# Kernel optimization log

Measured on AMD Instinct MI355X. Metric: run time of the kernel, lower is better.

Reference implementation:

```python
import jax, jax.numpy as jnp
import numpy as np

N_NODES, N_EDGES, N_GRAPHS = 20000, 320000, 8
NFD, HID, OUT, HEADS = 128, 64, 768, 4


def gat_conv(x, src, dst, ea, W, att_src, att_dst, We, att_edge, bias, heads, concat):
    """PyG GATConv with edge_dim, add_self_loops=True (fill_value='mean'), eval mode."""
    N = x.shape[0]
    H = heads
    C = W.shape[1] // H
    loop = jnp.arange(N, dtype=src.dtype)
    s = jnp.concatenate([src, loop])
    d = jnp.concatenate([dst, loop])
    ea_full = jnp.concatenate([ea, jnp.broadcast_to(ea.mean(axis=0), (N, ea.shape[1]))], axis=0)
    h = (x @ W).reshape(N, H, C)                      # [N,H,C]
    a_s = (h * att_src).sum(-1)                        # [N,H]
    a_d = (h * att_dst).sum(-1)                        # [N,H]
    eh = (ea_full @ We).reshape(-1, H, C)              # [Etot,H,C]
    a_e = (eh * att_edge).sum(-1)                      # [Etot,H]
    logit = jax.nn.leaky_relu(a_s[s] + a_d[d] + a_e, negative_slope=0.2)
    m = jax.ops.segment_max(logit, d, num_segments=N)  # segment softmax over dst
    w = jnp.exp(logit - m[d])
    z = jax.ops.segment_sum(w, d, num_segments=N)
    alpha = w / (z[d] + 1e-16)                         # [Etot,H]
    out = jax.ops.segment_sum(h[s] * alpha[:, :, None], d, num_segments=N)
    out = out.reshape(N, H * C) if concat else out.mean(axis=1)
    return out + bias


def setup_inputs() -> dict:
    key = jax.random.key(0)
    ks = jax.random.split(key, 32)
    p = lambda k, shp: (jax.random.normal(k, shp) * 0.1).astype(jnp.float32)
    inp = {
        'x': jax.random.normal(ks[0], (N_NODES, 5), dtype=jnp.float32),
        'edge_index': jax.random.randint(ks[1], (2, N_EDGES), 0, N_NODES, dtype=jnp.int32),
        'edge_attr': jax.random.uniform(ks[2], (N_EDGES, 4), dtype=jnp.float32),
        'batch': jnp.sort(jax.random.randint(ks[3], (N_NODES,), 0, N_GRAPHS, dtype=jnp.int32)),
        # node_encoder
        'enc_w1': p(ks[4], (5, NFD // 2)), 'enc_b1': jnp.zeros((NFD // 2,), jnp.float32),
        'enc_w2': p(ks[5], (NFD // 2, NFD)), 'enc_b2': jnp.zeros((NFD,), jnp.float32),
        # gat1: in NFD -> HEADS*HID (concat)
        'g1_w': p(ks[6], (NFD, HEADS * HID)), 'g1_asrc': p(ks[7], (HEADS, HID)),
        'g1_adst': p(ks[8], (HEADS, HID)), 'g1_we': p(ks[9], (4, HEADS * HID)),
        'g1_aedge': p(ks[10], (HEADS, HID)), 'g1_b': jnp.zeros((HEADS * HID,), jnp.float32),
        # gat2: in HEADS*HID -> HEADS*HID (concat)
        'g2_w': p(ks[11], (HEADS * HID, HEADS * HID)), 'g2_asrc': p(ks[12], (HEADS, HID)),
        'g2_adst': p(ks[13], (HEADS, HID)), 'g2_we': p(ks[14], (4, HEADS * HID)),
        'g2_aedge': p(ks[15], (HEADS, HID)), 'g2_b': jnp.zeros((HEADS * HID,), jnp.float32),
        # gat3: in HEADS*HID -> HID, heads=1, concat=False
        'g3_w': p(ks[16], (HEADS * HID, HID)), 'g3_asrc': p(ks[17], (1, HID)),
        'g3_adst': p(ks[18], (1, HID)), 'g3_we': p(ks[19], (4, HID)),
        'g3_aedge': p(ks[20], (1, HID)), 'g3_b': jnp.zeros((HID,), jnp.float32),
        # projection HID -> 2*HID -> OUT
        'proj_w1': p(ks[21], (HID, 2 * HID)), 'proj_b1': jnp.zeros((2 * HID,), jnp.float32),
        'proj_w2': p(ks[22], (2 * HID, OUT)), 'proj_b2': jnp.zeros((OUT,), jnp.float32),
        # 5 vulnerability heads stacked: OUT -> 5
        'vuln_w': p(ks[23], (OUT, 5)), 'vuln_b': jnp.zeros((5,), jnp.float32),
    }
    return inp


def reference(x, edge_index, edge_attr, batch,
              enc_w1, enc_b1, enc_w2, enc_b2,
              g1_w, g1_asrc, g1_adst, g1_we, g1_aedge, g1_b,
              g2_w, g2_asrc, g2_adst, g2_we, g2_aedge, g2_b,
              g3_w, g3_asrc, g3_adst, g3_we, g3_aedge, g3_b,
              proj_w1, proj_b1, proj_w2, proj_b2, vuln_w, vuln_b):
    src, dst = edge_index[0], edge_index[1]
    # node_encoder (eval mode, dropout = identity)
    h = jax.nn.relu(x @ enc_w1 + enc_b1)
    h = jax.nn.relu(h @ enc_w2 + enc_b2)                         # [N, NFD]
    # EdgeAwareGAT
    h = jax.nn.elu(gat_conv(h, src, dst, edge_attr, g1_w, g1_asrc, g1_adst, g1_we, g1_aedge, g1_b, HEADS, True))
    h = jax.nn.elu(gat_conv(h, src, dst, edge_attr, g2_w, g2_asrc, g2_adst, g2_we, g2_aedge, g2_b, HEADS, True))
    h = gat_conv(h, src, dst, edge_attr, g3_w, g3_asrc, g3_adst, g3_we, g3_aedge, g3_b, 1, False)  # [N, HID]
    # global_mean_pool
    sums = jax.ops.segment_sum(h, batch, num_segments=N_GRAPHS)
    cnts = jax.ops.segment_sum(jnp.ones((h.shape[0], 1), h.dtype), batch, num_segments=N_GRAPHS)
    g = sums / jnp.maximum(cnts, 1.0)                            # [B, HID]
    # projection
    p1 = jax.nn.relu(g @ proj_w1 + proj_b1)
    static_features = p1 @ proj_w2 + proj_b2                     # [B, OUT]
    scores = jax.nn.sigmoid(static_features @ vuln_w + vuln_b)   # [B, 5]
    return static_features, scores
```

## Files before the change

### kernel.cpp

```cpp
#include <hip/hip_runtime.h>
#include <hip/hip_bf16.h>
#include <hip/hip_fp16.h>
#include <math.h>

#define N_NODES 20000
#define M_PAD 20096
#define N_EDGES 320000
#define N_GRAPHS 8

typedef _Float16 half8 __attribute__((ext_vector_type(8)));
typedef float floatx4 __attribute__((ext_vector_type(4)));

struct h4pack { __half2 a, b; };

__device__ __forceinline__ float leaky02(float x) { return x > 0.f ? x : 0.2f * x; }
__device__ __forceinline__ float sel4(int hl, float a, float b, float c, float d) {
    return hl < 2 ? (hl == 0 ? a : b) : (hl == 2 ? c : d);
}

__global__ void encoder_kernel(const float* __restrict__ x,
                               const float* __restrict__ w1, const float* __restrict__ b1,
                               const float* __restrict__ w2, const float* __restrict__ b2,
                               __half* __restrict__ out) {
    const int n0 = blockIdx.x * 8;
    const int tid = threadIdx.x;
    __shared__ float s_x[8][5];
    __shared__ float s_h1[8][64];
    if (tid < 40) s_x[tid / 5][tid % 5] = x[(size_t)(n0 + tid / 5) * 5 + (tid % 5)];
    __syncthreads();
    if (tid < 64) {
        #pragma unroll
        for (int n = 0; n < 8; ++n) {
            float a = b1[tid];
            #pragma unroll
            for (int k = 0; k < 5; ++k) a += s_x[n][k] * w1[k * 64 + tid];
            s_h1[n][tid] = fmaxf(a, 0.f);
        }
    }
    __syncthreads();
    float acc[8];
    #pragma unroll
    for (int n = 0; n < 8; ++n) acc[n] = b2[tid];
    for (int k = 0; k < 64; ++k) {
        float wv = w2[k * 128 + tid];
        #pragma unroll
        for (int n = 0; n < 8; ++n) acc[n] += s_h1[n][k] * wv;
    }
    #pragma unroll
    for (int n = 0; n < 8; ++n)
        out[(size_t)(n0 + n) * 128 + tid] = __float2half(fmaxf(acc[n], 0.f));
}

__global__ void prep_kernel(const float* __restrict__ ea, const int* __restrict__ dst,
                            float* __restrict__ ea_sum, int* __restrict__ cnt) {
    const int tid = threadIdx.x;
    float a0 = 0, a1 = 0, a2 = 0, a3 = 0;
    for (int i = blockIdx.x * blockDim.x + tid; i < N_EDGES; i += gridDim.x * blockDim.x) {
        float4 v = ((const float4*)ea)[i];
        a0 += v.x; a1 += v.y; a2 += v.z; a3 += v.w;
        atomicAdd(&cnt[dst[i]], 1);
    }
    #pragma unroll
    for (int off = 32; off; off >>= 1) {
        a0 += __shfl_down(a0, off, 64);
        a1 += __shfl_down(a1, off, 64);
        a2 += __shfl_down(a2, off, 64);
        a3 += __shfl_down(a3, off, 64);
    }
    __shared__ float s[4][4];
    const int wave = tid >> 6, lane = tid & 63;
    if (lane == 0) { s[wave][0] = a0; s[wave][1] = a1; s[wave][2] = a2; s[wave][3] = a3; }
    __syncthreads();
    if (tid < 4) {
        float t = s[0][tid] + s[1][tid] + s[2][tid] + s[3][tid];
        atomicAdd(&ea_sum[tid], t);
    }
}

__global__ void scan_kernel(const int* __restrict__ cnt, int* __restrict__ row_ptr) {
    __shared__ int s_sum[1024];
    const int tid = threadIdx.x;
    int local[20];
    int run = 0;
    const int base = tid * 20;
    #pragma unroll
    for (int i = 0; i < 20; ++i) {
        int idx = base + i;
        int v = (idx < N_NODES) ? cnt[idx] : 0;
        run += v;
        local[i] = run;
    }
    s_sum[tid] = run;
    __syncthreads();
    for (int off = 1; off < 1024; off <<= 1) {
        int v = (tid >= off) ? s_sum[tid - off] : 0;
        __syncthreads();
        s_sum[tid] += v;
        __syncthreads();
    }
    const int prev = (tid > 0) ? s_sum[tid - 1] : 0;
    #pragma unroll
    for (int i = 0; i < 20; ++i) {
        int idx = base + i;
        if (idx < N_NODES) row_ptr[idx + 1] = prev + local[i];
    }
    if (tid == 0) row_ptr[0] = 0;
}

__global__ void scatter_kernel(const int* __restrict__ src, const int* __restrict__ dst,
                               const float* __restrict__ ea,
                               const int* __restrict__ row_ptr, int* __restrict__ cur,
                               int* __restrict__ csr_src, float* __restrict__ csr_ea) {
    int i = blockIdx.x * 256 + threadIdx.x;
    if (i < N_EDGES) {
        int d = dst[i];
        int p = atomicAdd(&cur[d], 1);
        int idx = row_ptr[d] + p;
        csr_src[idx] = src[i];
        ((float4*)csr_ea)[idx] = ((const float4*)ea)[i];
    }
}

__global__ void const_prep_kernel(const float* __restrict__ w1, const float* __restrict__ w2,
                                  const float* __restrict__ w3,
                                  __half* __restrict__ wt1, __half* __restrict__ wt2,
                                  __half* __restrict__ wt3,
                                  const float* __restrict__ we1, const float* __restrict__ ae1,
                                  const float* __restrict__ we2, const float* __restrict__ ae2,
                                  const float* __restrict__ we3, const float* __restrict__ ae3,
                                  const float* __restrict__ ea_sum,
                                  float* __restrict__ vtab, float* __restrict__ lpae) {
    const int b = blockIdx.x;
    if (b < 448) {
        int i = b * 256 + threadIdx.x;
        if (i < 32768) {
            int k = i >> 8, n = i & 255;
            wt1[(size_t)n * 128 + k] = __float2half(w1[i]);
        } else if (i < 98304) {
            int j = i - 32768;
            int k = j >> 8, n = j & 255;
            wt2[(size_t)n * 256 + k] = __float2half(w2[j]);
        } else if (i < 114688) {
            int j = i - 98304;
            int k = j >> 6, n = j & 63;
            wt3[(size_t)n * 256 + k] = __float2half(w3[j]);
        }
        return;
    }
    const int L = b - 448;
    const float* We = (L == 0) ? we1 : ((L == 1) ? we2 : we3);
    const float* Ae = (L == 0) ? ae1 : ((L == 1) ? ae2 : ae3);
    const int H = (L < 2) ? 4 : 1;
    const int tid = threadIdx.x;
    __shared__ float s_v[16];
    if (tid < 4 * H) {
        const int k = tid / H, h = tid % H;
        float v = 0.f;
        for (int c = 0; c < 64; ++c) v += We[k * (H * 64) + h * 64 + c] * Ae[h * 64 + c];
        vtab[L * 16 + k * 4 + h] = v;
        s_v[k * 4 + h] = v;
    }
    __syncthreads();
    if (tid < H) {
        const float inv = 1.0f / (float)N_EDGES;
        float l = 0.f;
        #pragma unroll
        for (int k = 0; k < 4; ++k) l += ea_sum[k] * inv * s_v[k * 4 + tid];
        lpae[L * 4 + tid] = l;
    }
}

template<int N, int H>
__global__ __launch_bounds__(256) void mgemm_kernel(
    const __half* __restrict__ X, const __half* __restrict__ Wt,
    const float* __restrict__ asrc, const float* __restrict__ adst,
    __half* __restrict__ Y, float* __restrict__ a_s, float* __restrict__ a_d, int K) {
    constexpr int STR = 72;
    __shared__ _Float16 sX[64 * STR];
    __shared__ _Float16 sW[64 * STR];
    const int tid = threadIdx.x;
    const int lane = tid & 63, w = tid >> 6;
    const int l16 = lane & 15, kg = lane >> 4;
    const int n0 = blockIdx.x * 64;
    const int c0 = blockIdx.y * 64;
    const int by = blockIdx.y;

    floatx4 acc[4];
    #pragma unroll
    for (int ct = 0; ct < 4; ++ct) acc[ct] = (floatx4){0.f, 0.f, 0.f, 0.f};

    const int srow = tid >> 2, sseg = tid & 3;
    for (int k0 = 0; k0 < K; k0 += 64) {
        float4 xv0 = *(const float4*)(X + (size_t)(n0 + srow) * K + k0 + sseg * 8);
        float4 xv1 = *(const float4*)(X + (size_t)(n0 + srow) * K + k0 + 32 + sseg * 8);
        float4 wv0 = *(const float4*)(Wt + (size_t)(c0 + srow) * K + k0 + sseg * 8);
        float4 wv1 = *(const float4*)(Wt + (size_t)(c0 + srow) * K + k0 + 32 + sseg * 8);
        __syncthreads();
        *(float4*)&sX[srow * STR + sseg * 8] = xv0;
        *(float4*)&sX[srow * STR + 32 + sseg * 8] = xv1;
        *(float4*)&sW[srow * STR + sseg * 8] = wv0;
        *(float4*)&sW[srow * STR + 32 + sseg * 8] = wv1;
        __syncthreads();
        #pragma unroll
        for (int ks = 0; ks < 2; ++ks) {
            half8 a = *(const half8*)&sX[(w * 16 + l16) * STR + ks * 32 + kg * 8];
            #pragma unroll
            for (int ct = 0; ct < 4; ++ct) {
                half8 b = *(const half8*)&sW[(ct * 16 + l16) * STR + ks * 32 + kg * 8];
                acc[ct] = __builtin_amdgcn_mfma_f32_16x16x32_f16(a, b, acc[ct], 0, 0, 0);
            }
        }
    }

    const int rowb = n0 + w * 16 + kg * 4;
    float ar[4], ad4[4];
    #pragma unroll
    for (int ct = 0; ct < 4; ++ct) {
        ar[ct] = asrc[c0 + ct * 16 + l16];
        ad4[ct] = adst[c0 + ct * 16 + l16];
    }
    #pragma unroll
    for (int ct = 0; ct < 4; ++ct) {
        const int col = c0 + ct * 16 + l16;
        #pragma unroll
        for (int r = 0; r < 4; ++r)
            Y[(size_t)(rowb + r) * N + col] = __float2half(acc[ct][r]);
    }
    #pragma unroll
    for (int r = 0; r < 4; ++r) {
        float p = acc[0][r] * ar[0] + acc[1][r] * ar[1] + acc[2][r] * ar[2] + acc[3][r] * ar[3];
        float q = acc[0][r] * ad4[0] + acc[1][r] * ad4[1] + acc[2][r] * ad4[2] + acc[3][r] * ad4[3];
        #pragma unroll
        for (int off = 1; off < 16; off <<= 1) {
            p += __shfl_xor(p, off, 64);
            q += __shfl_xor(q, off, 64);
        }
        if (l16 == 0) {
            const int node = rowb + r;
            a_s[(size_t)node * H + by] = p;
            a_d[(size_t)node * H + by] = q;
        }
    }
}

template<int H, int HC, bool ELU>
__global__ __launch_bounds__(256) void agg4_kernel(
    const __half* __restrict__ hh,
    const float* __restrict__ a_s, const float* __restrict__ a_d,
    const float* __restrict__ vtab, const float* __restrict__ lpae,
    const int* __restrict__ csr_src, const float* __restrict__ csr_ea,
    const int* __restrict__ row_ptr, const float* __restrict__ bias,
    __half* __restrict__ out) {
    constexpr int CPT = HC / 64;
    const int wave = threadIdx.x >> 6;
    const int lane = threadIdx.x & 63;
    const int d = blockIdx.x * 4 + wave;

    const int base = row_ptr[d], end = row_ptr[d + 1];
    const int colbase = lane * CPT;
    const int hl = (H == 1) ? 0 : (colbase >> 6);

    float vt[4][H];
    #pragma unroll
    for (int k = 0; k < 4; ++k)
        #pragma unroll
        for (int h = 0; h < H; ++h) vt[k][h] = vtab[k * 4 + h];

    float add_[H], lself[H];
    if (H == 4) {
        float4 t = *(const float4*)&a_d[(size_t)d * 4];
        add_[0] = t.x; add_[1] = t.y; add_[2] = t.z; add_[3] = t.w;
        float4 s4 = *(const float4*)&a_s[(size_t)d * 4];
        lself[0] = leaky02(s4.x + add_[0] + lpae[0]);
        lself[1] = leaky02(s4.y + add_[1] + lpae[1]);
        lself[2] = leaky02(s4.z + add_[2] + lpae[2]);
        lself[3] = leaky02(s4.w + add_[3] + lpae[3]);
    } else {
        add_[0] = a_d[d];
        lself[0] = leaky02(a_s[d] + add_[0] + lpae[0]);
    }

    float zacc = 1.f;
    float acc[CPT];
    if (CPT == 4) {
        h4pack hv = *(const h4pack*)(hh + (size_t)d * HC + colbase);
        float2 f0 = __half22float2(hv.a);
        float2 f1 = __half22float2(hv.b);
        acc[0] = f0.x; acc[1] = f0.y; acc[2] = f1.x; acc[3] = f1.y;
    } else {
        acc[0] = __half2float(hh[(size_t)d * HC + colbase]);
    }

#define EDGE_STEP(tt) { \
        int s_ = __shfl(my_s, (tt), 64); \
        float w_; \
        if (H == 4) { \
            float t0 = __shfl(w0, (tt), 64), t1 = __shfl(w1, (tt), 64); \
            float t2 = __shfl(w2, (tt), 64), t3 = __shfl(w3, (tt), 64); \
            w_ = sel4(hl, t0, t1, t2, t3); \
        } else { \
            w_ = __shfl(w0, (tt), 64); \
        } \
        if (CPT == 4) { \
            h4pack hv_ = *(const h4pack*)(hh + (size_t)s_ * HC + colbase); \
            float2 f0_ = __half22float2(hv_.a); \
            float2 f1_ = __half22float2(hv_.b); \
            acc[0] += w_ * f0_.x; acc[1] += w_ * f0_.y; \
            acc[2] += w_ * f1_.x; acc[3] += w_ * f1_.y; \
        } else { \
            acc[0] += w_ * __half2float(hh[(size_t)s_ * HC + colbase]); \
        } \
        zacc += w_; }

    for (int c0 = base; c0 < end; c0 += 64) {
        const int nc = min(64, end - c0);
        int my_s = 0;
        float w0 = 0.f, w1 = 0.f, w2 = 0.f, w3 = 0.f;
        if (lane < nc) {
            my_s = csr_src[c0 + lane];
            float4 eav = ((const float4*)csr_ea)[c0 + lane];
            if (H == 4) {
                float4 as4 = *(const float4*)&a_s[(size_t)my_s * 4];
                float l0 = leaky02(as4.x + add_[0] + eav.x * vt[0][0] + eav.y * vt[1][0] + eav.z * vt[2][0] + eav.w * vt[3][0]);
                float l1 = leaky02(as4.y + add_[1] + eav.x * vt[0][1] + eav.y * vt[1][1] + eav.z * vt[2][1] + eav.w * vt[3][1]);
                float l2 = leaky02(as4.z + add_[2] + eav.x * vt[0][2] + eav.y * vt[1][2] + eav.z * vt[2][2] + eav.w * vt[3][2]);
                float l3 = leaky02(as4.w + add_[3] + eav.x * vt[0][3] + eav.y * vt[1][3] + eav.z * vt[2][3] + eav.w * vt[3][3]);
                w0 = __expf(l0 - lself[0]);
                w1 = __expf(l1 - lself[1]);
                w2 = __expf(l2 - lself[2]);
                w3 = __expf(l3 - lself[3]);
            } else {
                float l0 = leaky02(a_s[my_s] + add_[0] + eav.x * vt[0][0] + eav.y * vt[1][0] + eav.z * vt[2][0] + eav.w * vt[3][0]);
                w0 = __expf(l0 - lself[0]);
            }
        }
        int t = 0;
        for (; t + 8 <= nc; t += 8) {
            EDGE_STEP(t)
            EDGE_STEP(t + 1)
            EDGE_STEP(t + 2)
            EDGE_STEP(t + 3)
            EDGE_STEP(t + 4)
            EDGE_STEP(t + 5)
            EDGE_STEP(t + 6)
            EDGE_STEP(t + 7)
        }
        for (; t < nc; ++t) {
            EDGE_STEP(t)
        }
    }
#undef EDGE_STEP

    const float invz = 1.f / (zacc + 1e-16f);
    #pragma unroll
    for (int c = 0; c < CPT; ++c) {
        float v = acc[c] * invz + bias[colbase + c];
        if (ELU) v = (v > 0.f) ? v : (__expf(v) - 1.f);
        acc[c] = v;
    }
    if (CPT == 4) {
        __half2* op = (__half2*)(out + (size_t)d * HC + colbase);
        op[0] = __floats2half2_rn(acc[0], acc[1]);
        op[1] = __floats2half2_rn(acc[2], acc[3]);
    } else {
        out[(size_t)d * HC + colbase] = __float2half(acc[0]);
    }
}

__global__ void pool_kernel(const __half* __restrict__ h3, const int* __restrict__ batch,
                            float* __restrict__ psum, float* __restrict__ pcnt) {
    __shared__ float s_acc[8][64];
    __shared__ float s_cnt[8];
    const int tid = threadIdx.x;
    for (int i = tid; i < 512; i += 256) s_acc[i >> 6][i & 63] = 0.f;
    if (tid < 8) s_cnt[tid] = 0.f;
    __syncthreads();
    const int col = tid & 63, nl = tid >> 6;
    const int n0 = blockIdx.x * 64;
    for (int nn = nl; nn < 64; nn += 4) {
        int n = n0 + nn;
        if (n < N_NODES) {
            int b = batch[n];
            atomicAdd(&s_acc[b][col], __half2float(h3[(size_t)n * 64 + col]));
            if (col == 0) atomicAdd(&s_cnt[b], 1.0f);
        }
    }
    __syncthreads();
    for (int i = tid; i < 512; i += 256) {
        float v = s_acc[i >> 6][i & 63];
        if (v != 0.f) atomicAdd(&psum[i], v);
    }
    if (tid < 8 && s_cnt[tid] > 0.f) atomicAdd(&pcnt[tid], s_cnt[tid]);
}

__global__ void head_sf_kernel(const float* __restrict__ psum, const float* __restrict__ pcnt,
                               const float* __restrict__ w1, const float* __restrict__ b1,
                               const float* __restrict__ w2, const float* __restrict__ b2,
                               float* __restrict__ out) {
    const int b = blockIdx.y;
    const int c0 = blockIdx.x * 128;
    const int tid = threadIdx.x;
    __shared__ float s_g[64];
    __shared__ float s_p1[128];
    if (tid < 64) {
        float c = pcnt[b];
        c = (c < 1.f) ? 1.f : c;
        s_g[tid] = psum[b * 64 + tid] / c;
    }
    __syncthreads();
    {
        float a = b1[tid];
        #pragma unroll 8
        for (int k = 0; k < 64; ++k) a += s_g[k] * w1[k * 128 + tid];
        s_p1[tid] = fmaxf(a, 0.f);
    }
    __syncthreads();
    const int col = c0 + tid;
    float a = b2[col];
    #pragma unroll 8
    for (int k = 0; k < 128; ++k) a += s_p1[k] * w2[k * 768 + col];
    out[b * 768 + col] = a;
}

__global__ void scores_kernel(const float* __restrict__ sf,
                              const float* __restrict__ vw, const float* __restrict__ vb,
                              float* __restrict__ out) {
    const int b = blockIdx.x;
    const int tid = threadIdx.x;
    const int wave = tid >> 6, lane = tid & 63;
    float part[5] = {0.f, 0.f, 0.f, 0.f, 0.f};
    for (int k = tid; k < 768; k += 256) {
        float s = sf[b * 768 + k];
        #pragma unroll
        for (int v = 0; v < 5; ++v) part[v] += s * vw[k * 5 + v];
    }
    #pragma unroll
    for (int v = 0; v < 5; ++v)
        #pragma unroll
        for (int off = 32; off; off >>= 1) part[v] += __shfl_down(part[v], off, 64);
    __shared__ float sred[4][5];
    if (lane == 0) {
        #pragma unroll
        for (int v = 0; v < 5; ++v) sred[wave][v] = part[v];
    }
    __syncthreads();
    if (tid < 5) {
        float a = vb[tid] + sred[0][tid] + sred[1][tid] + sred[2][tid] + sred[3][tid];
        out[6144 + b * 5 + tid] = 1.f / (1.f + __expf(-a));
    }
}

extern "C" void kernel_launch(void* const* d_in, const int* in_sizes, int n_in,
                              void* d_out, int out_size, void* d_ws, size_t ws_size,
                              hipStream_t stream) {
    const float* x       = (const float*)d_in[0];
    const int*   eidx    = (const int*)d_in[1];
    const float* ea      = (const float*)d_in[2];
    const int*   batch   = (const int*)d_in[3];
    const float* enc_w1  = (const float*)d_in[4];
    const float* enc_b1  = (const float*)d_in[5];
    const float* enc_w2  = (const float*)d_in[6];
    const float* enc_b2  = (const float*)d_in[7];
    const float* g1_w    = (const float*)d_in[8];
    const float* g1_asrc = (const float*)d_in[9];
    const float* g1_adst = (const float*)d_in[10];
    const float* g1_we   = (const float*)d_in[11];
    const float* g1_ae   = (const float*)d_in[12];
    const float* g1_b    = (const float*)d_in[13];
    const float* g2_w    = (const float*)d_in[14];
    const float* g2_asrc = (const float*)d_in[15];
    const float* g2_adst = (const float*)d_in[16];
    const float* g2_we   = (const float*)d_in[17];
    const float* g2_ae   = (const float*)d_in[18];
    const float* g2_b    = (const float*)d_in[19];
    const float* g3_w    = (const float*)d_in[20];
    const float* g3_asrc = (const float*)d_in[21];
    const float* g3_adst = (const float*)d_in[22];
    const float* g3_we   = (const float*)d_in[23];
    const float* g3_ae   = (const float*)d_in[24];
    const float* g3_b    = (const float*)d_in[25];
    const float* pw1     = (const float*)d_in[26];
    const float* pb1     = (const float*)d_in[27];
    const float* pw2     = (const float*)d_in[28];
    const float* pb2     = (const float*)d_in[29];
    const float* vw      = (const float*)d_in[30];
    const float* vb      = (const float*)d_in[31];

    const int* src = eidx;
    const int* dst = eidx + N_EDGES;

    __half* h16a = (__half*)d_ws;
    __half* h16b = h16a + (size_t)M_PAD * 256;
    __half* hh16 = h16b + (size_t)M_PAD * 256;
    __half* wt1  = hh16 + (size_t)M_PAD * 256;
    __half* wt2  = wt1 + 32768;
    __half* wt3  = wt2 + 65536;
    float* asb   = (float*)(wt3 + 16384);
    float* adb   = asb + (size_t)M_PAD * 4;
    float* zreg  = adb + (size_t)M_PAD * 4;
    float* ea_sum = zreg;
    float* psum   = zreg + 4;
    float* pcnt   = zreg + 516;
    float* vtab   = zreg + 524;
    float* lpae   = zreg + 572;
    int* icnt    = (int*)(zreg + 584);
    int* icur    = icnt + N_NODES;
    int* irow    = icur + N_NODES;
    int* csr_src = irow + N_NODES + 16;
    float* csr_ea = (float*)(csr_src + N_EDGES);

    hipMemsetAsync(zreg, 0, 584 * sizeof(float), stream);
    hipMemsetAsync(icnt, 0, 2 * N_NODES * sizeof(int), stream);

    prep_kernel<<<256, 256, 0, stream>>>(ea, dst, ea_sum, icnt);
    encoder_kernel<<<N_NODES / 8, 128, 0, stream>>>(x, enc_w1, enc_b1, enc_w2, enc_b2, h16a);
    scan_kernel<<<1, 1024, 0, stream>>>(icnt, irow);
    scatter_kernel<<<(N_EDGES + 255) / 256, 256, 0, stream>>>(src, dst, ea, irow, icur, csr_src, csr_ea);
    const_prep_kernel<<<451, 256, 0, stream>>>(g1_w, g2_w, g3_w, wt1, wt2, wt3,
                                               g1_we, g1_ae, g2_we, g2_ae, g3_we, g3_ae,
                                               ea_sum, vtab, lpae);

    mgemm_kernel<256, 4><<<dim3(M_PAD / 64, 4), 256, 0, stream>>>(h16a, wt1, g1_asrc, g1_adst, hh16, asb, adb, 128);
    agg4_kernel<4, 256, true><<<N_NODES / 4, 256, 0, stream>>>(hh16, asb, adb, vtab, lpae, csr_src, csr_ea, irow, g1_b, h16b);

    mgemm_kernel<256, 4><<<dim3(M_PAD / 64, 4), 256, 0, stream>>>(h16b, wt2, g2_asrc, g2_adst, hh16, asb, adb, 256);
    agg4_kernel<4, 256, true><<<N_NODES / 4, 256, 0, stream>>>(hh16, asb, adb, vtab + 16, lpae + 4, csr_src, csr_ea, irow, g2_b, h16a);

    mgemm_kernel<64, 1><<<dim3(M_PAD / 64, 1), 256, 0, stream>>>(h16a, wt3, g3_asrc, g3_adst, hh16, asb, adb, 256);
    agg4_kernel<1, 64, false><<<N_NODES / 4, 256, 0, stream>>>(hh16, asb, adb, vtab + 32, lpae + 8, csr_src, csr_ea, irow, g3_b, h16b);

    pool_kernel<<<(N_NODES + 63) / 64, 256, 0, stream>>>(h16b, batch, psum, pcnt);
    head_sf_kernel<<<dim3(6, 8), 128, 0, stream>>>(psum, pcnt, pw1, pb1, pw2, pb2, (float*)d_out);
    scores_kernel<<<8, 256, 0, stream>>>((float*)d_out, vw, vb, (float*)d_out);
}
```

Measured before the change: 321.7 us.

## Pack CSR edges into int4 with fp16 attrs, half-pack weights, fuse head kernels

After: 315.1 us. 1.02x faster.

```diff
diff --git a/kernel.cpp b/kernel.cpp
--- a/kernel.cpp
+++ b/kernel.cpp
@@ -14,9 +14,6 @@
 struct h4pack { __half2 a, b; };
 
 __device__ __forceinline__ float leaky02(float x) { return x > 0.f ? x : 0.2f * x; }
-__device__ __forceinline__ float sel4(int hl, float a, float b, float c, float d) {
-    return hl < 2 ? (hl == 0 ? a : b) : (hl == 2 ? c : d);
-}
 
 __global__ void encoder_kernel(const float* __restrict__ x,
                                const float* __restrict__ w1, const float* __restrict__ b1,
@@ -110,14 +107,21 @@
 __global__ void scatter_kernel(const int* __restrict__ src, const int* __restrict__ dst,
                                const float* __restrict__ ea,
                                const int* __restrict__ row_ptr, int* __restrict__ cur,
-                               int* __restrict__ csr_src, float* __restrict__ csr_ea) {
+                               int4* __restrict__ csr_edges) {
     int i = blockIdx.x * 256 + threadIdx.x;
     if (i < N_EDGES) {
         int d = dst[i];
         int p = atomicAdd(&cur[d], 1);
         int idx = row_ptr[d] + p;
-        csr_src[idx] = src[i];
-        ((float4*)csr_ea)[idx] = ((const float4*)ea)[i];
+        float4 e = ((const float4*)ea)[i];
+        __half2 h01 = __floats2half2_rn(e.x, e.y);
+        __half2 h23 = __floats2half2_rn(e.z, e.w);
+        int4 r;
+        r.x = src[i];
+        r.y = *(int*)&h01;
+        r.z = *(int*)&h23;
+        r.w = 0;
+        csr_edges[idx] = r;
     }
 }
 
@@ -244,11 +248,11 @@
 }
 
 template<int H, int HC, bool ELU>
-__global__ __launch_bounds__(256) void agg4_kernel(
+__global__ __launch_bounds__(256) void agg5_kernel(
     const __half* __restrict__ hh,
     const float* __restrict__ a_s, const float* __restrict__ a_d,
     const float* __restrict__ vtab, const float* __restrict__ lpae,
-    const int* __restrict__ csr_src, const float* __restrict__ csr_ea,
+    const int4* __restrict__ csr_edges,
     const int* __restrict__ row_ptr, const float* __restrict__ bias,
     __half* __restrict__ out) {
     constexpr int CPT = HC / 64;
@@ -295,9 +299,12 @@
         int s_ = __shfl(my_s, (tt), 64); \
         float w_; \
         if (H == 4) { \
-            float t0 = __shfl(w0, (tt), 64), t1 = __shfl(w1, (tt), 64); \
-            float t2 = __shfl(w2, (tt), 64), t3 = __shfl(w3, (tt), 64); \
-            w_ = sel4(hl, t0, t1, t2, t3); \
+            int t01 = __shfl(wp01, (tt), 64); \
+            int t23 = __shfl(wp23, (tt), 64); \
+            int selw = (hl < 2) ? t01 : t23; \
+            __half2 hpw = *(__half2*)&selw; \
+            float2 fw = __half22float2(hpw); \
+            w_ = (hl & 1) ? fw.y : fw.x; \
         } else { \
             w_ = __shfl(w0, (tt), 64); \
         } \
@@ -315,22 +322,27 @@
     for (int c0 = base; c0 < end; c0 += 64) {
         const int nc = min(64, end - c0);
         int my_s = 0;
-        float w0 = 0.f, w1 = 0.f, w2 = 0.f, w3 = 0.f;
+        int wp01 = 0, wp23 = 0;
+        float w0 = 0.f;
         if (lane < nc) {
-            my_s = csr_src[c0 + lane];
-            float4 eav = ((const float4*)csr_ea)[c0 + lane];
+            int4 er = csr_edges[c0 + lane];
+            my_s = er.x;
+            __half2 h01 = *(__half2*)&er.y;
+            __half2 h23 = *(__half2*)&er.z;
+            float2 e01 = __half22float2(h01);
+            float2 e23 = __half22float2(h23);
             if (H == 4) {
                 float4 as4 = *(const float4*)&a_s[(size_t)my_s * 4];
-                float l0 = leaky02(as4.x + add_[0] + eav.x * vt[0][0] + eav.y * vt[1][0] + eav.z * vt[2][0] + eav.w * vt[3][0]);
-                float l1 = leaky02(as4.y + add_[1] + eav.x * vt[0][1] + eav.y * vt[1][1] + eav.z * vt[2][1] + eav.w * vt[3][1]);
-                float l2 = leaky02(as4.z + add_[2] + eav.x * vt[0][2] + eav.y * vt[1][2] + eav.z * vt[2][2] + eav.w * vt[3][2]);
-                float l3 = leaky02(as4.w + add_[3] + eav.x * vt[0][3] + eav.y * vt[1][3] + eav.z * vt[2][3] + eav.w * vt[3][3]);
-                w0 = __expf(l0 - lself[0]);
-                w1 = __expf(l1 - lself[1]);
-                w2 = __expf(l2 - lself[2]);
-                w3 = __expf(l3 - lself[3]);
+                float l0 = leaky02(as4.x + add_[0] + e01.x * vt[0][0] + e01.y * vt[1][0] + e23.x * vt[2][0] + e23.y * vt[3][0]);
+                float l1 = leaky02(as4.y + add_[1] + e01.x * vt[0][1] + e01.y * vt[1][1] + e23.x * vt[2][1] + e23.y * vt[3][1]);
+                float l2 = leaky02(as4.z + add_[2] + e01.x * vt[0][2] + e01.y * vt[1][2] + e23.x * vt[2][2] + e23.y * vt[3][2]);
+                float l3 = leaky02(as4.w + add_[3] + e01.x * vt[0][3] + e01.y * vt[1][3] + e23.x * vt[2][3] + e23.y * vt[3][3]);
+                __half2 p01 = __floats2half2_rn(__expf(l0 - lself[0]), __expf(l1 - lself[1]));
+                __half2 p23 = __floats2half2_rn(__expf(l2 - lself[2]), __expf(l3 - lself[3]));
+                wp01 = *(int*)&p01;
+                wp23 = *(int*)&p23;
             } else {
-                float l0 = leaky02(a_s[my_s] + add_[0] + eav.x * vt[0][0] + eav.y * vt[1][0] + eav.z * vt[2][0] + eav.w * vt[3][0]);
+                float l0 = leaky02(a_s[my_s] + add_[0] + e01.x * vt[0][0] + e01.y * vt[1][0] + e23.x * vt[2][0] + e23.y * vt[3][0]);
                 w0 = __expf(l0 - lself[0]);
             }
         }
@@ -393,60 +405,52 @@
     if (tid < 8 && s_cnt[tid] > 0.f) atomicAdd(&pcnt[tid], s_cnt[tid]);
 }
 
-__global__ void head_sf_kernel(const float* __restrict__ psum, const float* __restrict__ pcnt,
-                               const float* __restrict__ w1, const float* __restrict__ b1,
-                               const float* __restrict__ w2, const float* __restrict__ b2,
-                               float* __restrict__ out) {
-    const int b = blockIdx.y;
-    const int c0 = blockIdx.x * 128;
-    const int tid = threadIdx.x;
+__global__ void head_kernel(const float* __restrict__ psum, const float* __restrict__ pcnt,
+                            const float* __restrict__ w1, const float* __restrict__ b1,
+                            const float* __restrict__ w2, const float* __restrict__ b2,
+                            const float* __restrict__ vw, const float* __restrict__ vb,
+                            float* __restrict__ out) {
+    const int b = blockIdx.x;
+    const int tid = threadIdx.x;
+    const int wave = tid >> 6, lane = tid & 63;
     __shared__ float s_g[64];
     __shared__ float s_p1[128];
+    __shared__ float s_red[12][5];
     if (tid < 64) {
         float c = pcnt[b];
         c = (c < 1.f) ? 1.f : c;
         s_g[tid] = psum[b * 64 + tid] / c;
     }
     __syncthreads();
-    {
+    if (tid < 128) {
         float a = b1[tid];
         #pragma unroll 8
         for (int k = 0; k < 64; ++k) a += s_g[k] * w1[k * 128 + tid];
         s_p1[tid] = fmaxf(a, 0.f);
     }
     __syncthreads();
-    const int col = c0 + tid;
-    float a = b2[col];
+    float a = b2[tid];
     #pragma unroll 8
-    for (int k = 0; k < 128; ++k) a += s_p1[k] * w2[k * 768 + col];
-    out[b * 768 + col] = a;
-}
-
-__global__ void scores_kernel(const float* __restrict__ sf,
-                              const float* __restrict__ vw, const float* __restrict__ vb,
-                              float* __restrict__ out) {
-    const int b = blockIdx.x;
-    const int tid = threadIdx.x;
-    const int wave = tid >> 6, lane = tid & 63;
-    float part[5] = {0.f, 0.f, 0.f, 0.f, 0.f};
-    for (int k = tid; k < 768; k += 256) {
-        float s = sf[b * 768 + k];
-        #pragma unroll
-        for (int v = 0; v < 5; ++v) part[v] += s * vw[k * 5 + v];
-    }
+    for (int k = 0; k < 128; ++k) a += s_p1[k] * w2[k * 768 + tid];
+    out[b * 768 + tid] = a;
+
+    float part[5];
+    #pragma unroll
+    for (int v = 0; v < 5; ++v) part[v] = a * vw[tid * 5 + v];
     #pragma unroll
     for (int v = 0; v < 5; ++v)
         #pragma unroll
         for (int off = 32; off; off >>= 1) part[v] += __shfl_down(part[v], off, 64);
-    __shared__ float sred[4][5];
     if (lane == 0) {
         #pragma unroll
-        for (int v = 0; v < 5; ++v) sred[wave][v] = part[v];
+        for (int v = 0; v < 5; ++v) s_red[wave][v] = part[v];
     }
     __syncthreads();
     if (tid < 5) {
-        float a = vb[tid] + sred[0][tid] + sred[1][tid] + sred[2][tid] + sred[3][tid];
-        out[6144 + b * 5 + tid] = 1.f / (1.f + __expf(-a));
+        float acc = vb[tid];
+        #pragma unroll
+        for (int w = 0; w < 12; ++w) acc += s_red[w][tid];
+        out[6144 + b * 5 + tid] = 1.f / (1.f + __expf(-acc));
     }
 }
 
@@ -506,8 +510,7 @@
     int* icnt    = (int*)(zreg + 584);
     int* icur    = icnt + N_NODES;
     int* irow    = icur + N_NODES;
-    int* csr_src = irow + N_NODES + 16;
-    float* csr_ea = (float*)(csr_src + N_EDGES);
+    int4* csr_edges = (int4*)(irow + N_NODES + 16);
 
     hipMemsetAsync(zreg, 0, 584 * sizeof(float), stream);
     hipMemsetAsync(icnt, 0, 2 * N_NODES * sizeof(int), stream);
@@ -515,21 +518,20 @@
     prep_kernel<<<256, 256, 0, stream>>>(ea, dst, ea_sum, icnt);
     encoder_kernel<<<N_NODES / 8, 128, 0, stream>>>(x, enc_w1, enc_b1, enc_w2, enc_b2, h16a);
     scan_kernel<<<1, 1024, 0, stream>>>(icnt, irow);
-    scatter_kernel<<<(N_EDGES + 255) / 256, 256, 0, stream>>>(src, dst, ea, irow, icur, csr_src, csr_ea);
+    scatter_kernel<<<(N_EDGES + 255) / 256, 256, 0, stream>>>(src, dst, ea, irow, icur, csr_edges);
     const_prep_kernel<<<451, 256, 0, stream>>>(g1_w, g2_w, g3_w, wt1, wt2, wt3,
                                                g1_we, g1_ae, g2_we, g2_ae, g3_we, g3_ae,
                                                ea_sum, vtab, lpae);
 
     mgemm_kernel<256, 4><<<dim3(M_PAD / 64, 4), 256, 0, stream>>>(h16a, wt1, g1_asrc, g1_adst, hh16, asb, adb, 128);
-    agg4_kernel<4, 256, true><<<N_NODES / 4, 256, 0, stream>>>(hh16, asb, adb, vtab, lpae, csr_src, csr_ea, irow, g1_b, h16b);
+    agg5_kernel<4, 256, true><<<N_NODES / 4, 256, 0, stream>>>(hh16, asb, adb, vtab, lpae, csr_edges, irow, g1_b, h16b);
 
     mgemm_kernel<256, 4><<<dim3(M_PAD / 64, 4), 256, 0, stream>>>(h16b, wt2, g2_asrc, g2_adst, hh16, asb, adb, 256);
-    agg4_kernel<4, 256, true><<<N_NODES / 4, 256, 0, stream>>>(hh16, asb, adb, vtab + 16, lpae + 4, csr_src, csr_ea, irow, g2_b, h16a);
+    agg5_kernel<4, 256, true><<<N_NODES / 4, 256, 0, stream>>>(hh16, asb, adb, vtab + 16, lpae + 4, csr_edges, irow, g2_b, h16a);
 
     mgemm_kernel<64, 1><<<dim3(M_PAD / 64, 1), 256, 0, stream>>>(h16a, wt3, g3_asrc, g3_adst, hh16, asb, adb, 256);
-    agg4_kernel<1, 64, false><<<N_NODES / 4, 256, 0, stream>>>(hh16, asb, adb, vtab + 32, lpae + 8, csr_src, csr_ea, irow, g3_b, h16b);
+    agg5_kernel<1, 64, false><<<N_NODES / 4, 256, 0, stream>>>(hh16, asb, adb, vtab + 32, lpae + 8, csr_edges, irow, g3_b, h16b);
 
     pool_kernel<<<(N_NODES + 63) / 64, 256, 0, stream>>>(h16b, batch, psum, pcnt);
-    head_sf_kernel<<<dim3(6, 8), 128, 0, stream>>>(psum, pcnt, pw1, pb1, pw2, pb2, (float*)d_out);
-    scores_kernel<<<8, 256, 0, stream>>>((float*)d_out, vw, vb, (float*)d_out);
-}
+    head_kernel<<<8, 768, 0, stream>>>(psum, pcnt, pw1, pb1, pw2, pb2, vw, vb, (float*)d_out);
+}
```
